# Kernel tuning notes

Hardware: AMD Instinct MI355X
Metric: run time of the kernel (lower is better)

The kernel has to match this reference:

```python
import jax, jax.numpy as jnp
import numpy as np

N, E, D, L, G = 50000, 625000, 128, 3, 64
EPS = 1e-5


def setup_inputs() -> dict:
    key = jax.random.key(0)
    ks = jax.random.split(key, 16)
    s = 1.0 / np.sqrt(D)
    inp = {
        "x": jax.random.normal(ks[0], (N, D), jnp.float32),
        "edge_index": jax.random.randint(ks[1], (2, E), 0, N, jnp.int64),
        "batch": jnp.sort(jax.random.randint(ks[2], (N,), 0, G, jnp.int64)),
        # node_emb
        "Wemb": jax.random.normal(ks[3], (D, D), jnp.float32) * s,
        "bemb": jnp.zeros((D,), jnp.float32),
        # per-layer params stacked on axis 0
        "Wscore": jax.random.normal(ks[4], (L, 1, D), jnp.float32) * s,
        "bscore": jnp.zeros((L, 1), jnp.float32),
        "Wfwd": jax.random.normal(ks[5], (L, D, D), jnp.float32) * s,
        "Wbwd": jax.random.normal(ks[6], (L, D, D), jnp.float32) * s,
        "Wself": jax.random.normal(ks[7], (L, D, D), jnp.float32) * s,
        "bself": jnp.zeros((L, D), jnp.float32),
        "Wcomb": jax.random.normal(ks[8], (L, D, 3 * D), jnp.float32) * s,
        "bcomb": jnp.zeros((L, D), jnp.float32),
        "gamma": jnp.ones((L, D), jnp.float32),
        "beta": jnp.zeros((L, D), jnp.float32),
    }
    return inp


def reference(x, edge_index, batch, Wemb, bemb, Wscore, bscore, Wfwd, Wbwd,
              Wself, bself, Wcomb, bcomb, gamma, beta):
    n = x.shape[0]
    src, dst = edge_index[0], edge_index[1]  # j (source), i (target)
    h = jax.nn.relu(x @ Wemb.T + bemb)       # dropout is eval-mode no-op
    for l in range(Wscore.shape[0]):
        identity = h
        scores = h @ Wscore[l].T + bscore[l]           # [N, 1]
        h_fwd = h @ Wfwd[l].T                          # [N, D]
        h_bwd = h @ Wbwd[l].T
        h_self = h @ Wself[l].T + bself[l]
        alpha = jax.nn.sigmoid(scores[src] - scores[dst])  # [E, 1]
        aggr_fwd = jax.ops.segment_sum(h_fwd[src] * alpha, dst, num_segments=n)
        aggr_bwd = jax.ops.segment_sum(h_bwd[src] * (1.0 - alpha), dst, num_segments=n)
        z = jnp.concatenate([h_self, aggr_fwd, aggr_bwd], axis=-1) @ Wcomb[l].T + bcomb[l]
        mu = jnp.mean(z, axis=-1, keepdims=True)
        var = jnp.var(z, axis=-1, keepdims=True)
        z = (z - mu) * jax.lax.rsqrt(var + EPS) * gamma[l] + beta[l]
        h = jax.nn.relu(z) + identity
    # global mean pool over graphs
    sums = jax.ops.segment_sum(h, batch, num_segments=G)
    cnt = jax.ops.segment_sum(jnp.ones((n,), h.dtype), batch, num_segments=G)
    return sums / jnp.maximum(cnt, 1.0)[:, None]
```

## Files before the change

### kernel.cpp

```cpp
#include <hip/hip_runtime.h>
#include <math.h>

#define EPS 1e-5f
#define PS 8
#define SW(row) (((row) & 7) << 4)

typedef __attribute__((ext_vector_type(8))) short short8;
typedef __attribute__((ext_vector_type(4))) float f32x4;

__device__ __forceinline__ float bf2f(unsigned short u) {
  union { unsigned i; float f; } c; c.i = ((unsigned)u) << 16; return c.f;
}
__device__ __forceinline__ float bflo(unsigned u) {
  union { unsigned i; float f; } c; c.i = u << 16; return c.f;
}
__device__ __forceinline__ float bfhi(unsigned u) {
  union { unsigned i; float f; } c; c.i = u & 0xFFFF0000u; return c.f;
}
__device__ __forceinline__ unsigned short f2bf(float f) {
  union { float f; unsigned i; } c; c.f = f;
  unsigned r = c.i + 0x7FFF + ((c.i >> 16) & 1);
  return (unsigned short)(r >> 16);
}

template <bool SCORE>
__global__ __launch_bounds__(256, 2) void embed_gemm(
    const float* __restrict__ X,
    const ushort* __restrict__ W,
    const float* __restrict__ bias,
    const float* __restrict__ Wsc, const float* __restrict__ bsc,
    ushort* __restrict__ hb, float* __restrict__ scores, int M) {
  __shared__ __align__(16) ushort As[64 * 128];
  __shared__ __align__(16) ushort Ws[128 * 128];
  __shared__ float lds3[64][2];

  const int t = threadIdx.x;
  const int lane = t & 63;
  const int w = t >> 6;
  const int wm = w >> 1, wn = w & 1;
  const int m0 = blockIdx.x * 64;
  const int l15 = lane & 15, l16 = lane >> 4;

  short8 ar[4], wr_[8];
#pragma unroll
  for (int it = 0; it < 4; ++it) {
    int chunk = it * 256 + t;
    int row = chunk >> 4;
    int b16 = chunk & 15;
    int grow = m0 + row; if (grow >= M) grow = M - 1;
    const float* xr = X + (size_t)grow * 128 + b16 * 8;
    float4 f0 = *(const float4*)xr;
    float4 f1 = *(const float4*)(xr + 4);
    short8 v;
    v[0] = (short)f2bf(f0.x); v[1] = (short)f2bf(f0.y);
    v[2] = (short)f2bf(f0.z); v[3] = (short)f2bf(f0.w);
    v[4] = (short)f2bf(f1.x); v[5] = (short)f2bf(f1.y);
    v[6] = (short)f2bf(f1.z); v[7] = (short)f2bf(f1.w);
    ar[it] = v;
  }
#pragma unroll
  for (int it = 0; it < 8; ++it) {
    int chunk = it * 256 + t;
    int row = chunk >> 4;
    int b16 = chunk & 15;
    wr_[it] = *(const short8*)(W + (size_t)row * 128 + b16 * 8);
  }
#pragma unroll
  for (int it = 0; it < 4; ++it) {
    int chunk = it * 256 + t;
    int row = chunk >> 4, b = (chunk & 15) * 16;
    *(short8*)((char*)As + row * 256 + (b ^ SW(row))) = ar[it];
  }
#pragma unroll
  for (int it = 0; it < 8; ++it) {
    int chunk = it * 256 + t;
    int row = chunk >> 4, b = (chunk & 15) * 16;
    *(short8*)((char*)Ws + row * 256 + (b ^ SW(row))) = wr_[it];
  }
  __syncthreads();

  f32x4 acc[2][4];
#pragma unroll
  for (int i = 0; i < 2; ++i)
#pragma unroll
    for (int j = 0; j < 4; ++j) acc[i][j] = (f32x4){0.f, 0.f, 0.f, 0.f};

#pragma unroll
  for (int kk = 0; kk < 4; ++kk) {
    int cb = kk * 64 + l16 * 16;
    short8 a[2], b[4];
#pragma unroll
    for (int i = 0; i < 2; ++i) {
      int row = wm * 32 + i * 16 + l15;
      a[i] = *(const short8*)((const char*)As + row * 256 + (cb ^ SW(row)));
    }
#pragma unroll
    for (int j = 0; j < 4; ++j) {
      int row = wn * 64 + j * 16 + l15;
      b[j] = *(const short8*)((const char*)Ws + row * 256 + (cb ^ SW(row)));
    }
#pragma unroll
    for (int i = 0; i < 2; ++i)
#pragma unroll
      for (int j = 0; j < 4; ++j)
        acc[i][j] = __builtin_amdgcn_mfma_f32_16x16x32_bf16(a[i], b[j], acc[i][j], 0, 0, 0);
  }

#pragma unroll
  for (int i = 0; i < 2; ++i)
#pragma unroll
    for (int r = 0; r < 4; ++r) {
      int row = m0 + wm * 32 + i * 16 + l16 * 4 + r;
      bool valid = row < M;
      float psc = 0.f;
#pragma unroll
      for (int j = 0; j < 4; ++j) {
        int colw = wn * 64 + j * 16 + l15;
        float v = acc[i][j][r] + bias[colw];
        v = fmaxf(v, 0.f);
        if (valid) hb[(size_t)row * 128 + colw] = f2bf(v);
        if (SCORE) psc += v * Wsc[colw];
      }
      if (SCORE) {
#pragma unroll
        for (int mm = 1; mm <= 8; mm <<= 1) psc += __shfl_xor(psc, mm, 64);
        if (l15 == 0) lds3[wm * 32 + i * 16 + l16 * 4 + r][wn] = psc;
      }
    }
  if (SCORE) {
    __syncthreads();
    if (wn == 0 && l15 == 0) {
#pragma unroll
      for (int i = 0; i < 2; ++i)
#pragma unroll
        for (int r = 0; r < 4; ++r) {
          int rl = wm * 32 + i * 16 + l16 * 4 + r;
          int row = blockIdx.x * 64 + rl;
          if (row < M) scores[row] = lds3[rl][0] + lds3[rl][1] + bsc[0];
        }
    }
  }
}

template <bool SCORE>
__global__ __launch_bounds__(256, 2) void layer_gemm(
    const ushort* __restrict__ A0,
    const ushort* __restrict__ A1,
    const ushort* __restrict__ W,
    const float* __restrict__ bias,
    const float* __restrict__ gamma, const float* __restrict__ beta,
    const float* __restrict__ Wsc, const float* __restrict__ bsc,
    ushort* __restrict__ hb, float* __restrict__ scores, int M) {
  __shared__ __align__(16) ushort As[64 * 192];
  __shared__ __align__(16) ushort Ws[128 * 192];
  __shared__ float lds1[64][2];
  __shared__ float lds2[64][2];
  __shared__ float lds3[64][2];

  const int t = threadIdx.x;
  const int lane = t & 63;
  const int w = t >> 6;
  const int wm = w >> 1, wn = w & 1;
  const int m0 = blockIdx.x * 64;
  const int l15 = lane & 15, l16 = lane >> 4;

  f32x4 acc[2][4];
#pragma unroll
  for (int i = 0; i < 2; ++i)
#pragma unroll
    for (int j = 0; j < 4; ++j) acc[i][j] = (f32x4){0.f, 0.f, 0.f, 0.f};

#pragma unroll
  for (int hf = 0; hf < 2; ++hf) {
    short8 ar[6], wr_[12];
#pragma unroll
    for (int it = 0; it < 6; ++it) {
      int chunk = it * 256 + t;
      int row = chunk / 24;
      int b16 = chunk % 24;
      int ec = hf * 192 + b16 * 8;
      int grow = m0 + row; if (grow >= M) grow = M - 1;
      const ushort* src = (ec < 128) ? (A0 + (size_t)grow * 128 + ec)
                                     : (A1 + (size_t)grow * 256 + (ec - 128));
      ar[it] = *(const short8*)src;
    }
#pragma unroll
    for (int it = 0; it < 12; ++it) {
      int chunk = it * 256 + t;
      int row = chunk / 24;
      int b16 = chunk % 24;
      wr_[it] = *(const short8*)(W + (size_t)row * 384 + hf * 192 + b16 * 8);
    }
    __syncthreads();
#pragma unroll
    for (int it = 0; it < 6; ++it) {
      int chunk = it * 256 + t;
      int row = chunk / 24, b = (chunk % 24) * 16;
      *(short8*)((char*)As + row * 384 + (b ^ SW(row))) = ar[it];
    }
#pragma unroll
    for (int it = 0; it < 12; ++it) {
      int chunk = it * 256 + t;
      int row = chunk / 24, b = (chunk % 24) * 16;
      *(short8*)((char*)Ws + row * 384 + (b ^ SW(row))) = wr_[it];
    }
    __syncthreads();
#pragma unroll
    for (int kk = 0; kk < 6; ++kk) {
      int cb = kk * 64 + l16 * 16;
      short8 a[2], b[4];
#pragma unroll
      for (int i = 0; i < 2; ++i) {
        int row = wm * 32 + i * 16 + l15;
        a[i] = *(const short8*)((const char*)As + row * 384 + (cb ^ SW(row)));
      }
#pragma unroll
      for (int j = 0; j < 4; ++j) {
        int row = wn * 64 + j * 16 + l15;
        b[j] = *(const short8*)((const char*)Ws + row * 384 + (cb ^ SW(row)));
      }
#pragma unroll
      for (int i = 0; i < 2; ++i)
#pragma unroll
        for (int j = 0; j < 4; ++j)
          acc[i][j] = __builtin_amdgcn_mfma_f32_16x16x32_bf16(a[i], b[j], acc[i][j], 0, 0, 0);
    }
  }

#pragma unroll
  for (int i = 0; i < 2; ++i)
#pragma unroll
    for (int r = 0; r < 4; ++r) {
      float p1 = 0.f, p2 = 0.f;
#pragma unroll
      for (int j = 0; j < 4; ++j) {
        int colw = wn * 64 + j * 16 + l15;
        float v = acc[i][j][r] + bias[colw];
        acc[i][j][r] = v;
        p1 += v;
        p2 += v * v;
      }
#pragma unroll
      for (int mm = 1; mm <= 8; mm <<= 1) {
        p1 += __shfl_xor(p1, mm, 64);
        p2 += __shfl_xor(p2, mm, 64);
      }
      if (l15 == 0) {
        int rl = wm * 32 + i * 16 + l16 * 4 + r;
        lds1[rl][wn] = p1;
        lds2[rl][wn] = p2;
      }
    }
  __syncthreads();
#pragma unroll
  for (int i = 0; i < 2; ++i)
#pragma unroll
    for (int r = 0; r < 4; ++r) {
      int rl = wm * 32 + i * 16 + l16 * 4 + r;
      int row = m0 + rl;
      bool valid = row < M;
      float s1 = lds1[rl][0] + lds1[rl][1];
      float s2 = lds2[rl][0] + lds2[rl][1];
      float mu = s1 * (1.f / 128.f);
      float var = s2 * (1.f / 128.f) - mu * mu;
      float rs = rsqrtf(var + EPS);
      float psc = 0.f;
#pragma unroll
      for (int j = 0; j < 4; ++j) {
        int colw = wn * 64 + j * 16 + l15;
        float v = acc[i][j][r];
        float o = (v - mu) * rs * gamma[colw] + beta[colw];
        o = fmaxf(o, 0.f);
        float res = o;
        if (valid) {
          res = o + bf2f(hb[(size_t)row * 128 + colw]);
          hb[(size_t)row * 128 + colw] = f2bf(res);
        }
        if (SCORE) psc += res * Wsc[colw];
      }
      if (SCORE) {
#pragma unroll
        for (int mm = 1; mm <= 8; mm <<= 1) psc += __shfl_xor(psc, mm, 64);
        if (l15 == 0) lds3[rl][wn] = psc;
      }
    }
  if (SCORE) {
    __syncthreads();
    if (wn == 0 && l15 == 0) {
#pragma unroll
      for (int i = 0; i < 2; ++i)
#pragma unroll
        for (int r = 0; r < 4; ++r) {
          int rl = wm * 32 + i * 16 + l16 * 4 + r;
          int row = m0 + rl;
          if (row < M) scores[row] = lds3[rl][0] + lds3[rl][1] + bsc[0];
        }
    }
  }
}

__global__ __launch_bounds__(256) void wpre_kernel(
    const float* __restrict__ Wcomb, const float* __restrict__ Wself,
    const float* __restrict__ Wfwd, const float* __restrict__ Wbwd,
    ushort* __restrict__ Wbig) {
  const int l = blockIdx.x / 3, p = blockIdx.x % 3;
  const float* Wc = Wcomb + (size_t)l * 128 * 384;
  const float* Wp = (p == 0 ? Wself : (p == 1 ? Wfwd : Wbwd)) + (size_t)l * 128 * 128;
  __shared__ float Bs[128][132];
  const int t = threadIdx.x;
  for (int i = t; i < 16384; i += 256) Bs[i >> 7][i & 127] = Wp[i];
  __syncthreads();
  const int r = t >> 1;
  const int c0 = (t & 1) * 64;
  float acc[64];
#pragma unroll
  for (int c = 0; c < 64; ++c) acc[c] = 0.f;
  for (int k = 0; k < 128; ++k) {
    float a = Wc[(size_t)r * 384 + p * 128 + k];
#pragma unroll
    for (int c4 = 0; c4 < 16; ++c4) {
      float4 b4 = *(const float4*)&Bs[k][c0 + c4 * 4];
      acc[c4 * 4 + 0] = fmaf(a, b4.x, acc[c4 * 4 + 0]);
      acc[c4 * 4 + 1] = fmaf(a, b4.y, acc[c4 * 4 + 1]);
      acc[c4 * 4 + 2] = fmaf(a, b4.z, acc[c4 * 4 + 2]);
      acc[c4 * 4 + 3] = fmaf(a, b4.w, acc[c4 * 4 + 3]);
    }
  }
  ushort* o = Wbig + (size_t)l * 128 * 384 + (size_t)r * 384 + p * 128 + c0;
#pragma unroll
  for (int c = 0; c < 64; ++c) o[c] = f2bf(acc[c]);
}

__global__ void bpre_kernel(const float* __restrict__ Wcomb, const float* __restrict__ bself,
                            const float* __restrict__ bcomb, float* __restrict__ biasc, int L) {
  int idx = blockIdx.x * 128 + threadIdx.x;
  if (idx >= L * 128) return;
  int l = idx >> 7;
  const float* Wc = Wcomb + (size_t)l * 128 * 384 + (size_t)(idx & 127) * 384;
  const float* bs = bself + (size_t)l * 128;
  float acc = bcomb[idx];
  for (int k = 0; k < 128; ++k) acc = fmaf(Wc[k], bs[k], acc);
  biasc[idx] = acc;
}

__global__ void f2b_kernel(const float* __restrict__ in, ushort* __restrict__ out, int n4) {
  int i = blockIdx.x * 256 + threadIdx.x;
  if (i < n4) {
    float4 v = ((const float4*)in)[i];
    ushort4 o;
    o.x = f2bf(v.x); o.y = f2bf(v.y); o.z = f2bf(v.z); o.w = f2bf(v.w);
    ((ushort4*)out)[i] = o;
  }
}

__global__ void hist_kernel(const int* __restrict__ dst, int* __restrict__ counts, int E) {
  int e = blockIdx.x * 256 + threadIdx.x;
  if (e < E) atomicAdd(&counts[dst[e]], 1);
}

__global__ __launch_bounds__(256) void scan1_kernel(
    const int* __restrict__ c, int* __restrict__ ex, int* __restrict__ partials, int n) {
  __shared__ int sd[256];
  int t = threadIdx.x, b = blockIdx.x;
  int base = b * 1024 + t * 4;
  int v0 = (base + 0 < n) ? c[base + 0] : 0;
  int v1 = (base + 1 < n) ? c[base + 1] : 0;
  int v2 = (base + 2 < n) ? c[base + 2] : 0;
  int v3 = (base + 3 < n) ? c[base + 3] : 0;
  int tot = v0 + v1 + v2 + v3;
  sd[t] = tot;
  __syncthreads();
  for (int off = 1; off < 256; off <<= 1) {
    int x = (t >= off) ? sd[t - off] : 0;
    __syncthreads();
    sd[t] += x;
    __syncthreads();
  }
  int p = sd[t] - tot;
  if (base + 0 < n) ex[base + 0] = p;
  if (base + 1 < n) ex[base + 1] = p + v0;
  if (base + 2 < n) ex[base + 2] = p + v0 + v1;
  if (base + 3 < n) ex[base + 3] = p + v0 + v1 + v2;
  if (t == 255) partials[b] = sd[255];
}

__global__ __launch_bounds__(256) void scan2_kernel(int* __restrict__ partials, int nb) {
  __shared__ int sd[256];
  int t = threadIdx.x;
  int v = (t < nb) ? partials[t] : 0;
  sd[t] = v;
  __syncthreads();
  for (int off = 1; off < 256; off <<= 1) {
    int x = (t >= off) ? sd[t - off] : 0;
    __syncthreads();
    sd[t] += x;
    __syncthreads();
  }
  if (t < nb) partials[t] = sd[t] - v;
}

__global__ void scan3_kernel(const int* __restrict__ ex, const int* __restrict__ partials,
                             int* __restrict__ indptr, int n, int E) {
  int i = blockIdx.x * 256 + threadIdx.x;
  if (i < n) indptr[i] = ex[i] + partials[i >> 10];
  if (i == 0) indptr[n] = E;
}

__global__ void scatter_kernel(const int* __restrict__ ei, int* __restrict__ cursor,
                               int* __restrict__ ssrc, int E) {
  int e = blockIdx.x * 256 + threadIdx.x;
  if (e >= E) return;
  int s = ei[e];
  int d = ei[E + e];
  int pos = atomicAdd(&cursor[d], 1);
  ssrc[pos] = s;
}

__global__ __launch_bounds__(256) void aggr_kernel(
    const int* __restrict__ indptr, const int* __restrict__ ssrc,
    const float* __restrict__ scores, const ushort* __restrict__ hb,
    ushort* __restrict__ uv, int Nn) {
  int node = blockIdx.x * 4 + (threadIdx.x >> 6);
  if (node >= Nn) return;
  int lane = threadIdx.x & 63;
  int beg = indptr[node], end = indptr[node + 1];
  float si = scores[node];
  float u0 = 0.f, u1 = 0.f, t0 = 0.f, t1 = 0.f;
  for (int ebase = beg; ebase < end; ebase += 64) {
    int cnt = min(64, end - ebase);
    int sv = 0;
    float al = 0.f;
    if (lane < cnt) {
      sv = ssrc[ebase + lane];
      al = 1.f / (1.f + __expf(si - scores[sv]));
    }
    int e = 0;
    for (; e + 4 <= cnt; e += 4) {
      int s0 = __shfl(sv, e, 64),     s1 = __shfl(sv, e + 1, 64);
      int s2 = __shfl(sv, e + 2, 64), s3 = __shfl(sv, e + 3, 64);
      float a0 = __shfl(al, e, 64),     a1 = __shfl(al, e + 1, 64);
      float a2 = __shfl(al, e + 2, 64), a3 = __shfl(al, e + 3, 64);
      unsigned v0 = *(const unsigned*)(hb + (size_t)s0 * 128 + lane * 2);
      unsigned v1 = *(const unsigned*)(hb + (size_t)s1 * 128 + lane * 2);
      unsigned v2 = *(const unsigned*)(hb + (size_t)s2 * 128 + lane * 2);
      unsigned v3 = *(const unsigned*)(hb + (size_t)s3 * 128 + lane * 2);
      float f;
      f = bflo(v0); u0 = fmaf(a0, f, u0); t0 += f;
      f = bfhi(v0); u1 = fmaf(a0, f, u1); t1 += f;
      f = bflo(v1); u0 = fmaf(a1, f, u0); t0 += f;
      f = bfhi(v1); u1 = fmaf(a1, f, u1); t1 += f;
      f = bflo(v2); u0 = fmaf(a2, f, u0); t0 += f;
      f = bfhi(v2); u1 = fmaf(a2, f, u1); t1 += f;
      f = bflo(v3); u0 = fmaf(a3, f, u0); t0 += f;
      f = bfhi(v3); u1 = fmaf(a3, f, u1); t1 += f;
    }
    for (; e < cnt; ++e) {
      int s_e = __shfl(sv, e, 64);
      float a_e = __shfl(al, e, 64);
      unsigned vv = *(const unsigned*)(hb + (size_t)s_e * 128 + lane * 2);
      float f0 = bflo(vv), f1 = bfhi(vv);
      u0 = fmaf(a_e, f0, u0); t0 += f0;
      u1 = fmaf(a_e, f1, u1); t1 += f1;
    }
  }
  unsigned pu = (unsigned)f2bf(u0) | ((unsigned)f2bf(u1) << 16);
  unsigned pv = (unsigned)f2bf(t0 - u0) | ((unsigned)f2bf(t1 - u1) << 16);
  *(unsigned*)(uv + (size_t)node * 256 + lane * 2) = pu;
  *(unsigned*)(uv + (size_t)node * 256 + 128 + lane * 2) = pv;
}

__global__ __launch_bounds__(128) void pool_stage_kernel(
    const ushort* __restrict__ hb, const int* __restrict__ batch,
    float* __restrict__ partial, int M) {
  int g = blockIdx.x, s = blockIdx.y, d = threadIdx.x;
  int lo = 0, hi = M;
  while (lo < hi) { int mid = (lo + hi) >> 1; if (batch[mid] < g) lo = mid + 1; else hi = mid; }
  int b0 = lo;
  hi = M;
  while (lo < hi) { int mid = (lo + hi) >> 1; if (batch[mid] <= g) lo = mid + 1; else hi = mid; }
  int b1 = lo;
  int len = b1 - b0;
  int chunk = (len + PS - 1) / PS;
  int r0 = b0 + s * chunk;
  int r1 = min(b1, r0 + chunk);
  float acc = 0.f;
  for (int i = r0; i < r1; ++i) acc += bf2f(hb[(size_t)i * 128 + d]);
  partial[((size_t)g * PS + s) * 128 + d] = acc;
}

__global__ void pool_final_kernel(const float* __restrict__ partial,
                                  const int* __restrict__ batch,
                                  float* __restrict__ out, int M, int G) {
  int idx = blockIdx.x * 256 + threadIdx.x;
  if (idx >= G * 128) return;
  int g = idx >> 7, d = idx & 127;
  float acc = 0.f;
#pragma unroll
  for (int s = 0; s < PS; ++s) acc += partial[((size_t)g * PS + s) * 128 + d];
  int lo = 0, hi = M;
  while (lo < hi) { int mid = (lo + hi) >> 1; if (batch[mid] < g) lo = mid + 1; else hi = mid; }
  int b0 = lo;
  hi = M;
  while (lo < hi) { int mid = (lo + hi) >> 1; if (batch[mid] <= g) lo = mid + 1; else hi = mid; }
  int c = lo - b0;
  out[idx] = acc / (float)(c > 0 ? c : 1);
}

extern "C" void kernel_launch(void* const* d_in, const int* in_sizes, int n_in,
                              void* d_out, int out_size, void* d_ws, size_t ws_size,
                              hipStream_t stream) {
  const float* x      = (const float*)d_in[0];
  const int*   ei     = (const int*)d_in[1];
  const int*   batch  = (const int*)d_in[2];
  const float* Wemb   = (const float*)d_in[3];
  const float* bemb   = (const float*)d_in[4];
  const float* Wscore = (const float*)d_in[5];
  const float* bscore = (const float*)d_in[6];
  const float* Wfwd   = (const float*)d_in[7];
  const float* Wbwd   = (const float*)d_in[8];
  const float* Wself  = (const float*)d_in[9];
  const float* bself  = (const float*)d_in[10];
  const float* Wcomb  = (const float*)d_in[11];
  const float* bcomb  = (const float*)d_in[12];
  const float* gamma  = (const float*)d_in[13];
  const float* beta   = (const float*)d_in[14];

  const int N = in_sizes[0] / 128;
  const int E = in_sizes[1] / 2;
  const int L = in_sizes[5] / 128;
  const int G = out_size / 128;
  float* out = (float*)d_out;

  char* p = (char*)d_ws;
  auto alloc = [&](size_t bytes) -> char* {
    char* r = p;
    p += (bytes + 255) & ~(size_t)255;
    return r;
  };
  ushort* hb16   = (ushort*)alloc((size_t)N * 128 * 2);
  ushort* uv     = (ushort*)alloc((size_t)N * 256 * 2);
  float*  scores = (float*)alloc((size_t)N * 4);
  ushort* Wemb_b = (ushort*)alloc(16384 * 2);
  ushort* Wbig   = (ushort*)alloc((size_t)L * 128 * 384 * 2);
  float*  biasc  = (float*)alloc((size_t)L * 128 * 4);
  int* counts    = (int*)alloc((size_t)N * 4);
  int* ex        = (int*)alloc((size_t)N * 4);
  int* partials  = (int*)alloc(1024);
  int* indptr    = (int*)alloc((size_t)(N + 1) * 4);
  int* cursor    = (int*)alloc((size_t)N * 4);
  int* ssrc      = (int*)alloc((size_t)E * 4);
  float* pool_p  = (float*)alloc((size_t)G * PS * 128 * 4);

  const int gb = (N + 63) / 64;

  f2b_kernel<<<16, 256, 0, stream>>>(Wemb, Wemb_b, 4096);
  wpre_kernel<<<3 * L, 256, 0, stream>>>(Wcomb, Wself, Wfwd, Wbwd, Wbig);
  bpre_kernel<<<L, 128, 0, stream>>>(Wcomb, bself, bcomb, biasc, L);

  hipMemsetAsync(counts, 0, (size_t)N * 4, stream);
  hist_kernel<<<(E + 255) / 256, 256, 0, stream>>>(ei + E, counts, E);
  int nb = (N + 1023) / 1024;
  scan1_kernel<<<nb, 256, 0, stream>>>(counts, ex, partials, N);
  scan2_kernel<<<1, 256, 0, stream>>>(partials, nb);
  scan3_kernel<<<(N + 255) / 256, 256, 0, stream>>>(ex, partials, indptr, N, E);
  hipMemcpyAsync(cursor, indptr, (size_t)N * 4, hipMemcpyDeviceToDevice, stream);
  scatter_kernel<<<(E + 255) / 256, 256, 0, stream>>>(ei, cursor, ssrc, E);

  embed_gemm<true><<<gb, 256, 0, stream>>>(x, Wemb_b, bemb, Wscore, bscore,
                                           hb16, scores, N);

  for (int l = 0; l < L; ++l) {
    aggr_kernel<<<(N + 3) / 4, 256, 0, stream>>>(indptr, ssrc, scores, hb16, uv, N);
    if (l < L - 1) {
      layer_gemm<true><<<gb, 256, 0, stream>>>(
          hb16, uv, Wbig + (size_t)l * 128 * 384, biasc + (size_t)l * 128,
          gamma + (size_t)l * 128, beta + (size_t)l * 128,
          Wscore + (size_t)(l + 1) * 128, bscore + (l + 1), hb16, scores, N);
    } else {
      layer_gemm<false><<<gb, 256, 0, stream>>>(
          hb16, uv, Wbig + (size_t)l * 128 * 384, biasc + (size_t)l * 128,
          gamma + (size_t)l * 128, beta + (size_t)l * 128,
          nullptr, nullptr, hb16, scores, N);
    }
  }

  pool_stage_kernel<<<dim3(G, PS), 128, 0, stream>>>(hb16, batch, pool_p, N);
  pool_final_kernel<<<(G * 128 + 255) / 256, 256, 0, stream>>>(pool_p, batch, out, N, G);
}
```

Before: 433.0 us.

## Use 16-lane groups per node with 16-byte gathers in aggregation; fuse cursor copy

The aggregation kernel now assigns a quarter-wavefront (16 lanes) to each node instead of a full wavefront, so each lane gathers 8 bf16 values with one 16-byte load rather than 2 with a 4-byte load. This aims to cut the number of memory instructions and idle lanes for low-degree nodes, where the average degree is about 12. The cost is more accumulator registers per lane. Separately, scan3 now writes the cursor array directly, which removes a device-to-device memcpy.

```diff
diff --git a/kernel.cpp b/kernel.cpp
--- a/kernel.cpp
+++ b/kernel.cpp
@@ -400,9 +400,14 @@
 }
 
 __global__ void scan3_kernel(const int* __restrict__ ex, const int* __restrict__ partials,
-                             int* __restrict__ indptr, int n, int E) {
+                             int* __restrict__ indptr, int* __restrict__ cursor,
+                             int n, int E) {
   int i = blockIdx.x * 256 + threadIdx.x;
-  if (i < n) indptr[i] = ex[i] + partials[i >> 10];
+  if (i < n) {
+    int v = ex[i] + partials[i >> 10];
+    indptr[i] = v;
+    cursor[i] = v;
+  }
   if (i == 0) indptr[n] = E;
 }
 
@@ -420,53 +425,72 @@
     const int* __restrict__ indptr, const int* __restrict__ ssrc,
     const float* __restrict__ scores, const ushort* __restrict__ hb,
     ushort* __restrict__ uv, int Nn) {
-  int node = blockIdx.x * 4 + (threadIdx.x >> 6);
+  const int t = threadIdx.x;
+  const int lane = t & 63;
+  const int q = lane & 15;
+  const int qbase = lane & 48;
+  const int node = blockIdx.x * 16 + (t >> 6) * 4 + (lane >> 4);
   if (node >= Nn) return;
-  int lane = threadIdx.x & 63;
   int beg = indptr[node], end = indptr[node + 1];
   float si = scores[node];
-  float u0 = 0.f, u1 = 0.f, t0 = 0.f, t1 = 0.f;
-  for (int ebase = beg; ebase < end; ebase += 64) {
-    int cnt = min(64, end - ebase);
+  float u0 = 0.f, u1 = 0.f, u2 = 0.f, u3 = 0.f;
+  float u4 = 0.f, u5 = 0.f, u6 = 0.f, u7 = 0.f;
+  float t0 = 0.f, t1 = 0.f, t2 = 0.f, t3 = 0.f;
+  float t4 = 0.f, t5 = 0.f, t6 = 0.f, t7 = 0.f;
+
+  for (int ebase = beg; ebase < end; ebase += 16) {
+    int cnt = min(16, end - ebase);
     int sv = 0;
     float al = 0.f;
-    if (lane < cnt) {
-      sv = ssrc[ebase + lane];
+    if (q < cnt) {
+      sv = ssrc[ebase + q];
       al = 1.f / (1.f + __expf(si - scores[sv]));
     }
     int e = 0;
     for (; e + 4 <= cnt; e += 4) {
-      int s0 = __shfl(sv, e, 64),     s1 = __shfl(sv, e + 1, 64);
-      int s2 = __shfl(sv, e + 2, 64), s3 = __shfl(sv, e + 3, 64);
-      float a0 = __shfl(al, e, 64),     a1 = __shfl(al, e + 1, 64);
-      float a2 = __shfl(al, e + 2, 64), a3 = __shfl(al, e + 3, 64);
-      unsigned v0 = *(const unsigned*)(hb + (size_t)s0 * 128 + lane * 2);
-      unsigned v1 = *(const unsigned*)(hb + (size_t)s1 * 128 + lane * 2);
-      unsigned v2 = *(const unsigned*)(hb + (size_t)s2 * 128 + lane * 2);
-      unsigned v3 = *(const unsigned*)(hb + (size_t)s3 * 128 + lane * 2);
+      int s0 = __shfl(sv, qbase + e, 64),     s1 = __shfl(sv, qbase + e + 1, 64);
+      int s2 = __shfl(sv, qbase + e + 2, 64), s3 = __shfl(sv, qbase + e + 3, 64);
+      float a0 = __shfl(al, qbase + e, 64),     a1 = __shfl(al, qbase + e + 1, 64);
+      float a2 = __shfl(al, qbase + e + 2, 64), a3 = __shfl(al, qbase + e + 3, 64);
+      uint4 v0 = *(const uint4*)(hb + (size_t)s0 * 128 + q * 8);
+      uint4 v1 = *(const uint4*)(hb + (size_t)s1 * 128 + q * 8);
+      uint4 v2 = *(const uint4*)(hb + (size_t)s2 * 128 + q * 8);
+      uint4 v3 = *(const uint4*)(hb + (size_t)s3 * 128 + q * 8);
       float f;
-      f = bflo(v0); u0 = fmaf(a0, f, u0); t0 += f;
-      f = bfhi(v0); u1 = fmaf(a0, f, u1); t1 += f;
-      f = bflo(v1); u0 = fmaf(a1, f, u0); t0 += f;
-      f = bfhi(v1); u1 = fmaf(a1, f, u1); t1 += f;
-      f = bflo(v2); u0 = fmaf(a2, f, u0); t0 += f;
-      f = bfhi(v2); u1 = fmaf(a2, f, u1); t1 += f;
-      f = bflo(v3); u0 = fmaf(a3, f, u0); t0 += f;
-      f = bfhi(v3); u1 = fmaf(a3, f, u1); t1 += f;
+#define ACC8(V, A)                                              \
+      f = bflo(V.x); u0 = fmaf(A, f, u0); t0 += f;              \
+      f = bfhi(V.x); u1 = fmaf(A, f, u1); t1 += f;              \
+      f = bflo(V.y); u2 = fmaf(A, f, u2); t2 += f;              \
+      f = bfhi(V.y); u3 = fmaf(A, f, u3); t3 += f;              \
+      f = bflo(V.z); u4 = fmaf(A, f, u4); t4 += f;              \
+      f = bfhi(V.z); u5 = fmaf(A, f, u5); t5 += f;              \
+      f = bflo(V.w); u6 = fmaf(A, f, u6); t6 += f;              \
+      f = bfhi(V.w); u7 = fmaf(A, f, u7); t7 += f;
+      ACC8(v0, a0)
+      ACC8(v1, a1)
+      ACC8(v2, a2)
+      ACC8(v3, a3)
     }
     for (; e < cnt; ++e) {
-      int s_e = __shfl(sv, e, 64);
-      float a_e = __shfl(al, e, 64);
-      unsigned vv = *(const unsigned*)(hb + (size_t)s_e * 128 + lane * 2);
-      float f0 = bflo(vv), f1 = bfhi(vv);
-      u0 = fmaf(a_e, f0, u0); t0 += f0;
-      u1 = fmaf(a_e, f1, u1); t1 += f1;
-    }
-  }
-  unsigned pu = (unsigned)f2bf(u0) | ((unsigned)f2bf(u1) << 16);
-  unsigned pv = (unsigned)f2bf(t0 - u0) | ((unsigned)f2bf(t1 - u1) << 16);
-  *(unsigned*)(uv + (size_t)node * 256 + lane * 2) = pu;
-  *(unsigned*)(uv + (size_t)node * 256 + 128 + lane * 2) = pv;
+      int s_e = __shfl(sv, qbase + e, 64);
+      float a_e = __shfl(al, qbase + e, 64);
+      uint4 vv = *(const uint4*)(hb + (size_t)s_e * 128 + q * 8);
+      float f;
+      ACC8(vv, a_e)
+#undef ACC8
+    }
+  }
+  uint4 pu, pv;
+  pu.x = (unsigned)f2bf(u0) | ((unsigned)f2bf(u1) << 16);
+  pu.y = (unsigned)f2bf(u2) | ((unsigned)f2bf(u3) << 16);
+  pu.z = (unsigned)f2bf(u4) | ((unsigned)f2bf(u5) << 16);
+  pu.w = (unsigned)f2bf(u6) | ((unsigned)f2bf(u7) << 16);
+  pv.x = (unsigned)f2bf(t0 - u0) | ((unsigned)f2bf(t1 - u1) << 16);
+  pv.y = (unsigned)f2bf(t2 - u2) | ((unsigned)f2bf(t3 - u3) << 16);
+  pv.z = (unsigned)f2bf(t4 - u4) | ((unsigned)f2bf(t5 - u5) << 16);
+  pv.w = (unsigned)f2bf(t6 - u6) | ((unsigned)f2bf(t7 - u7) << 16);
+  *(uint4*)(uv + (size_t)node * 256 + q * 8) = pu;
+  *(uint4*)(uv + (size_t)node * 256 + 128 + q * 8) = pv;
 }
 
 __global__ __launch_bounds__(128) void pool_stage_kernel(
@@ -562,15 +586,14 @@
   int nb = (N + 1023) / 1024;
   scan1_kernel<<<nb, 256, 0, stream>>>(counts, ex, partials, N);
   scan2_kernel<<<1, 256, 0, stream>>>(partials, nb);
-  scan3_kernel<<<(N + 255) / 256, 256, 0, stream>>>(ex, partials, indptr, N, E);
-  hipMemcpyAsync(cursor, indptr, (size_t)N * 4, hipMemcpyDeviceToDevice, stream);
+  scan3_kernel<<<(N + 255) / 256, 256, 0, stream>>>(ex, partials, indptr, cursor, N, E);
   scatter_kernel<<<(E + 255) / 256, 256, 0, stream>>>(ei, cursor, ssrc, E);
 
   embed_gemm<true><<<gb, 256, 0, stream>>>(x, Wemb_b, bemb, Wscore, bscore,
                                            hb16, scores, N);
 
   for (int l = 0; l < L; ++l) {
-    aggr_kernel<<<(N + 3) / 4, 256, 0, stream>>>(indptr, ssrc, scores, hb16, uv, N);
+    aggr_kernel<<<(N + 15) / 16, 256, 0, stream>>>(indptr, ssrc, scores, hb16, uv, N);
     if (l < L - 1) {
       layer_gemm<true><<<gb, 256, 0, stream>>>(
           hb16, uv, Wbig + (size_t)l * 128 * 384, biasc + (size_t)l * 128,
```

After: 425.4 us. Within noise of the previous version (-1.7%).
